# Optimization experiments

Hardware: AMD Instinct MI355X
Metric: run time of the kernel (lower is better)

## Reference

```python
import jax, jax.numpy as jnp
import numpy as np

N, D_IN, D_HID, D_OUT = 16384, 512, 2048, 512
NUM_BANDS, RANK, ALPHA = 4, 16, 32
SCALING = ALPHA / RANK  # 2.0


def setup_inputs() -> dict:
    key = jax.random.key(0)
    ks = jax.random.split(key, 10)
    x = jax.random.normal(ks[0], (N, D_IN), dtype=jnp.float32)
    bw = jax.random.uniform(ks[1], (N, NUM_BANDS), dtype=jnp.float32)
    band_weights = bw / jnp.sum(bw, axis=-1, keepdims=True)  # rows sum to 1
    s_in = 1.0 / np.sqrt(D_IN)
    s_hid = 1.0 / np.sqrt(D_HID)
    return {
        "x": x,
        "band_weights": band_weights,
        "W1": jax.random.normal(ks[2], (D_IN, D_HID), dtype=jnp.float32) * s_in,
        "b1": jax.random.normal(ks[3], (D_HID,), dtype=jnp.float32) * 0.01,
        "W2": jax.random.normal(ks[4], (D_HID, D_OUT), dtype=jnp.float32) * s_hid,
        "b2": jax.random.normal(ks[5], (D_OUT,), dtype=jnp.float32) * 0.01,
        "lora_fc1_A": jax.random.normal(ks[6], (NUM_BANDS, D_IN, RANK), dtype=jnp.float32) * s_in,
        "lora_fc1_B": jax.random.normal(ks[7], (NUM_BANDS, RANK, D_HID), dtype=jnp.float32) * 0.02,
        "lora_fc2_A": jax.random.normal(ks[8], (NUM_BANDS, D_HID, RANK), dtype=jnp.float32) * s_hid,
        "lora_fc2_B": jax.random.normal(ks[9], (NUM_BANDS, RANK, D_OUT), dtype=jnp.float32) * 0.02,
    }


def reference(x, band_weights, W1, b1, W2, b2, lora_fc1_A, lora_fc1_B, lora_fc2_A, lora_fc2_B):
    # shared fc1: [N, hidden]
    h_shared = x @ W1 + b1
    # per-band LoRA down-projection: [N, bands, rank]
    t1 = jnp.einsum('ni,bir->nbr', x, lora_fc1_A)
    # up-project and band-weighted sum fused: [N, hidden]
    delta1 = jnp.einsum('nb,nbr,brh->nh', band_weights, t1, lora_fc1_B) * SCALING
    h = jax.nn.gelu(h_shared + delta1, approximate=False)  # torch GELU is erf-based
    out_shared = h @ W2 + b2
    t2 = jnp.einsum('nh,bhr->nbr', h, lora_fc2_A)
    delta2 = jnp.einsum('nb,nbr,bro->no', band_weights, t2, lora_fc2_B) * SCALING
    return out_shared + delta2
```

## Files before the change

### kernel.cpp

```cpp
#include <hip/hip_runtime.h>
#include <hip/hip_bf16.h>

#define DEV __device__ __forceinline__
#define AS1 __attribute__((address_space(1)))
#define AS3 __attribute__((address_space(3)))

typedef __attribute__((ext_vector_type(8))) short bf16x8;
typedef __attribute__((ext_vector_type(4))) float f32x4;

static constexpr int NR   = 16384;
static constexpr int DIN  = 512;
static constexpr int DHID = 2048;
static constexpr int DOUT = 512;
static constexpr int LR   = 64;
static constexpr int K1   = DIN + LR;
static constexpr int K2   = DHID + LR;

DEV unsigned short f2bf(float f) {
  unsigned u = __float_as_uint(f);
  u += 0x7fffu + ((u >> 16) & 1u);
  return (unsigned short)(u >> 16);
}

DEV float fast_gelu(float v) {
  float x2 = v * v;
  float a  = -v * __builtin_fmaf(0.10294324f, x2, 2.30220817f);
  float t  = exp2f(a);
  return v * __builtin_amdgcn_rcpf(1.0f + t);
}

template<int N> DEV void wvm() {
  asm volatile("s_waitcnt vmcnt(%0)" :: "i"(N) : "memory");
}

__global__ __launch_bounds__(256) void cvt_x_kernel(const float* __restrict__ x,
                                                    unsigned short* __restrict__ xaug) {
  int i = blockIdx.x * 256 + threadIdx.x;
  if (i >= NR * DIN / 4) return;
  int e = i * 4;
  int r = e >> 9, c = e & 511;
  float4 v = ((const float4*)x)[i];
  uint2 o;
  o.x = (unsigned)f2bf(v.x) | ((unsigned)f2bf(v.y) << 16);
  o.y = (unsigned)f2bf(v.z) | ((unsigned)f2bf(v.w) << 16);
  *(uint2*)(xaug + (size_t)r * K1 + c) = o;
}

template<int R, int C, int LDO, int CO>
__global__ __launch_bounds__(256) void tconv_kernel(const float* __restrict__ in,
                                                    unsigned short* __restrict__ out) {
  __shared__ float t[32][33];
  int bc = blockIdx.x * 32, br = blockIdx.y * 32;
  int tx = threadIdx.x & 31, ty = threadIdx.x >> 5;
  #pragma unroll
  for (int i = 0; i < 32; i += 8)
    t[ty + i][tx] = in[(size_t)(br + ty + i) * C + bc + tx];
  __syncthreads();
  #pragma unroll
  for (int i = 0; i < 32; i += 8)
    out[(size_t)(bc + ty + i) * LDO + CO + br + tx] = f2bf(t[tx][ty + i]);
}

__global__ __launch_bounds__(256) void rearrA_kernel(const float* __restrict__ A,
                                                     unsigned short* __restrict__ AT, int D) {
  int tid = blockIdx.x * 256 + threadIdx.x;
  if (tid >= 64 * D) return;
  int j = tid / D, i = tid - j * D;
  AT[tid] = f2bf(A[((size_t)(j >> 4) * D + i) * 16 + (j & 15)]);
}

template<int BM, int BN, int WAVES, int K, int EPI>
__global__ __launch_bounds__(WAVES * 64, 2) void gemmx_kernel(
    const unsigned short* __restrict__ A, int lda,
    const unsigned short* __restrict__ B, int ldb,
    const float* __restrict__ bias,
    void* __restrict__ outp, int ldo, int ocol) {
  constexpr int THREADS = WAVES * 64;
  constexpr int NT = K / 64;
  constexpr int AL = BM * 4 / THREADS;
  constexpr int BL = BN * 4 / THREADS;
  constexpr int HA = (BM / 2) * 64;
  constexpr int HB = (BN / 2) * 64;
  constexpr int MQ = BM / 64;
  constexpr int WC = WAVES / 2;
  static_assert(NT >= 2 && AL == 2 && BL == 2, "geometry");
  __shared__ __align__(16) unsigned short lA[4 * HA];
  __shared__ __align__(16) unsigned short lB[4 * HB];

  const int tid  = threadIdx.x;
  const int w    = tid >> 6, lane = tid & 63;
  const int wr   = w / WC, wc = w % WC;
  const int bm   = blockIdx.x * BM, bn = blockIdx.y * BN;
  const int l15  = lane & 15;
  const int kc0  = ((lane >> 4) ^ (lane & 7)) * 8;
  const int kc1  = (((lane >> 4) + 4) ^ (lane & 7)) * 8;

  f32x4 acc[2][2][MQ][2] = {};
  bf16x8 af[2][MQ][2];
  bf16x8 bfv[2][2];

  auto stageA = [&](int buf, int half, int t) {
    #pragma unroll
    for (int i = 0; i < AL; ++i) {
      int row = w * (AL * 8) + i * 8 + (lane >> 3);
      __builtin_amdgcn_global_load_lds(
          (const AS1 void*)(A + (size_t)(bm + half * (BM / 2) + row) * lda
                              + (size_t)t * 64 + (((lane & 7) ^ (row & 7)) * 8)),
          (AS3 void*)(lA + (buf * 2 + half) * HA + (w * AL + i) * 512),
          16, 0, 0);
    }
  };
  auto stageB = [&](int buf, int half, int t) {
    #pragma unroll
    for (int i = 0; i < BL; ++i) {
      int row = w * (BL * 8) + i * 8 + (lane >> 3);
      __builtin_amdgcn_global_load_lds(
          (const AS1 void*)(B + (size_t)(bn + half * (BN / 2) + row) * ldb
                              + (size_t)t * 64 + (((lane & 7) ^ (row & 7)) * 8)),
          (AS3 void*)(lB + (buf * 2 + half) * HB + (w * BL + i) * 512),
          16, 0, 0);
    }
  };
  auto ldAall = [&](int buf) {
    #pragma unroll
    for (int mh = 0; mh < 2; ++mh) {
      const unsigned short* sA = lA + (buf * 2 + mh) * HA;
      #pragma unroll
      for (int m = 0; m < MQ; ++m) {
        int ro = (wr * (BM / 4) + m * 16 + l15) * 64;
        af[mh][m][0] = *(const bf16x8*)(sA + ro + kc0);
        af[mh][m][1] = *(const bf16x8*)(sA + ro + kc1);
      }
    }
  };
  auto ldB = [&](int buf, int nh) {
    const unsigned short* sB = lB + (buf * 2 + nh) * HB;
    #pragma unroll
    for (int n = 0; n < 2; ++n) {
      int ro = (wc * 32 + n * 16 + l15) * 64;
      bfv[n][0] = *(const bf16x8*)(sB + ro + kc0);
      bfv[n][1] = *(const bf16x8*)(sB + ro + kc1);
    }
  };

#define MFMA_Q(mh, nh)                                                           \
  __builtin_amdgcn_s_setprio(1);                                                 \
  _Pragma("unroll")                                                              \
  for (int m = 0; m < MQ; ++m)                                                   \
    _Pragma("unroll")                                                            \
    for (int n = 0; n < 2; ++n) {                                                \
      acc[mh][nh][m][n] = __builtin_amdgcn_mfma_f32_16x16x32_bf16(               \
          af[mh][m][0], bfv[n][0], acc[mh][nh][m][n], 0, 0, 0);                  \
      acc[mh][nh][m][n] = __builtin_amdgcn_mfma_f32_16x16x32_bf16(               \
          af[mh][m][1], bfv[n][1], acc[mh][nh][m][n], 0, 0, 0);                  \
    }                                                                            \
  __builtin_amdgcn_s_setprio(0);

#define BAR() __builtin_amdgcn_s_barrier()

  stageA(0, 0, 0); stageA(0, 1, 0); stageB(0, 0, 0); stageB(0, 1, 0);
  wvm<2>();
  BAR();

  for (int t = 0; t < NT; ++t) {
    const int buf = t & 1, nb = buf ^ 1;
    const bool more = (t + 1 < NT);
    ldAall(buf);
    ldB(buf, 0);
    if (more) { stageA(nb, 0, t + 1); stageA(nb, 1, t + 1); stageB(nb, 0, t + 1); }
    MFMA_Q(0, 0);
    MFMA_Q(1, 0);
    if (more) wvm<6>(); else wvm<0>();
    BAR();
    if (more) stageB(nb, 1, t + 1);
    ldB(buf, 1);
    MFMA_Q(0, 1);
    MFMA_Q(1, 1);
    if (more) {
      wvm<2>();
      BAR();
    }
  }
#undef MFMA_Q
#undef BAR

  float biasv[2][2];
  #pragma unroll
  for (int nh = 0; nh < 2; ++nh)
    #pragma unroll
    for (int n = 0; n < 2; ++n)
      biasv[nh][n] = bias[bn + nh * (BN / 2) + wc * 32 + n * 16 + l15];

  #pragma unroll
  for (int mh = 0; mh < 2; ++mh)
    #pragma unroll
    for (int nh = 0; nh < 2; ++nh)
      #pragma unroll
      for (int m = 0; m < MQ; ++m)
        #pragma unroll
        for (int n = 0; n < 2; ++n) {
          int col  = bn + nh * (BN / 2) + wc * 32 + n * 16 + l15;
          int rowb = bm + mh * (BM / 2) + wr * (BM / 4) + m * 16 + ((lane >> 4) << 2);
          #pragma unroll
          for (int r = 0; r < 4; ++r) {
            float v = acc[mh][nh][m][n][r];
            int row = rowb + r;
            if (EPI == 0) {
              v = fast_gelu(v + biasv[nh][n]);
              ((unsigned short*)outp)[(size_t)row * ldo + ocol + col] = f2bf(v);
            } else {
              v += biasv[nh][n];
              ((float*)outp)[(size_t)row * ldo + col] = v;
            }
          }
        }
}

template<int BM, int BN, int WM, int WN, int K>
__global__ __launch_bounds__(256) void gemmu_kernel(
    const unsigned short* __restrict__ A, int lda,
    const unsigned short* __restrict__ B, int ldb,
    const float* __restrict__ bw,
    unsigned short* __restrict__ outp, int ldo, int ocol) {
  constexpr int WRM = WM / 16, WRN = WN / 16;
  constexpr int NWN = BN / WN;
  constexpr int NT  = K / 64;
  constexpr int NBUF = 3;
  constexpr int AISS = BM * 64 * 2 / 4096;
  constexpr int BISS = BN * 64 * 2 / 4096;
  constexpr int LOADS = AISS + BISS;
  static_assert((BM / WM) * (BN / WN) == 4 && NT >= NBUF, "geometry");
  __shared__ __align__(16) unsigned short lA[NBUF * BM * 64];
  __shared__ __align__(16) unsigned short lB[NBUF * BN * 64];

  const int tid  = threadIdx.x;
  const int wid  = tid >> 6, lane = tid & 63;
  const int wr   = wid / NWN, wc = wid % NWN;
  const int bm   = blockIdx.x * BM, bn = blockIdx.y * BN;
  const int l15  = lane & 15;
  const int kc0  = ((lane >> 4) ^ (lane & 7)) * 8;
  const int kc1  = (((lane >> 4) + 4) ^ (lane & 7)) * 8;

  f32x4 acc[WRM][WRN] = {};

  auto stage = [&](int buf, int t) {
    #pragma unroll
    for (int i = 0; i < AISS; i++) {
      int row = (wid * AISS + i) * 8 + (lane >> 3);
      __builtin_amdgcn_global_load_lds(
          (const AS1 void*)(A + (size_t)(bm + row) * lda + (size_t)t * 64
                              + (((lane & 7) ^ (row & 7)) * 8)),
          (AS3 void*)(lA + buf * (BM * 64) + (wid * AISS + i) * 512), 16, 0, 0);
    }
    #pragma unroll
    for (int i = 0; i < BISS; i++) {
      int row = (wid * BISS + i) * 8 + (lane >> 3);
      __builtin_amdgcn_global_load_lds(
          (const AS1 void*)(B + (size_t)(bn + row) * ldb + (size_t)t * 64
                              + (((lane & 7) ^ (row & 7)) * 8)),
          (AS3 void*)(lB + buf * (BN * 64) + (wid * BISS + i) * 512), 16, 0, 0);
    }
  };
  auto compute = [&](int buf) {
    const unsigned short* pA = lA + buf * (BM * 64);
    const unsigned short* pB = lB + buf * (BN * 64);
    bf16x8 af[WRM][2], bfv[WRN][2];
    #pragma unroll
    for (int m = 0; m < WRM; m++) {
      int ro = (wr * WM + m * 16 + l15) * 64;
      af[m][0] = *(const bf16x8*)(pA + ro + kc0);
      af[m][1] = *(const bf16x8*)(pA + ro + kc1);
    }
    #pragma unroll
    for (int n = 0; n < WRN; n++) {
      int ro = (wc * WN + n * 16 + l15) * 64;
      bfv[n][0] = *(const bf16x8*)(pB + ro + kc0);
      bfv[n][1] = *(const bf16x8*)(pB + ro + kc1);
    }
    #pragma unroll
    for (int m = 0; m < WRM; m++)
      #pragma unroll
      for (int n = 0; n < WRN; n++) {
        acc[m][n] = __builtin_amdgcn_mfma_f32_16x16x32_bf16(af[m][0], bfv[n][0], acc[m][n], 0, 0, 0);
        acc[m][n] = __builtin_amdgcn_mfma_f32_16x16x32_bf16(af[m][1], bfv[n][1], acc[m][n], 0, 0, 0);
      }
  };

  stage(0, 0); stage(1, 1); stage(2, 2);
  wvm<2 * LOADS>();
  __builtin_amdgcn_s_barrier();

  int bt = 0;
  for (int t = 0; t < NT; ++t) {
    compute(bt);
    __builtin_amdgcn_s_barrier();
    if (t + 1 < NT) {
      if (t + NBUF < NT) stage(bt, t + NBUF);
      int newer = (t + NBUF < NT) ? (NBUF - 1) : (NT - 2 - t);
      if (newer >= 2)      wvm<2 * LOADS>();
      else if (newer == 1) wvm<LOADS>();
      else                 wvm<0>();
      __builtin_amdgcn_s_barrier();
      bt = (bt == NBUF - 1) ? 0 : bt + 1;
    }
  }

  const int r0 = bm + wr * WM;
  const int c0 = bn + wc * WN;
  #pragma unroll
  for (int m = 0; m < WRM; m++)
    #pragma unroll
    for (int n = 0; n < WRN; n++) {
      int col  = c0 + n * 16 + l15;
      int rowb = r0 + m * 16 + ((lane >> 4) << 2);
      #pragma unroll
      for (int r = 0; r < 4; r++) {
        float v = acc[m][n][r] * 2.0f * bw[(rowb + r) * 4 + (col >> 4)];
        outp[(size_t)(rowb + r) * ldo + ocol + col] = f2bf(v);
      }
    }
}

extern "C" void kernel_launch(void* const* d_in, const int* in_sizes, int n_in,
                              void* d_out, int out_size, void* d_ws, size_t ws_size,
                              hipStream_t stream) {
  const float* x  = (const float*)d_in[0];
  const float* bw = (const float*)d_in[1];
  const float* W1 = (const float*)d_in[2];
  const float* b1 = (const float*)d_in[3];
  const float* W2 = (const float*)d_in[4];
  const float* b2 = (const float*)d_in[5];
  const float* A1 = (const float*)d_in[6];
  const float* B1 = (const float*)d_in[7];
  const float* A2 = (const float*)d_in[8];
  const float* B2 = (const float*)d_in[9];
  float* out = (float*)d_out;

  char* w = (char*)d_ws;
  unsigned short* xaug = (unsigned short*)w;  w += (size_t)NR * K1 * 2;
  unsigned short* haug = (unsigned short*)w;  w += (size_t)NR * K2 * 2;
  unsigned short* W1cT = (unsigned short*)w;  w += (size_t)DHID * K1 * 2;
  unsigned short* W2cT = (unsigned short*)w;  w += (size_t)DOUT * K2 * 2;
  unsigned short* A1T  = (unsigned short*)w;  w += (size_t)64 * DIN * 2;
  unsigned short* A2T  = (unsigned short*)w;  w += (size_t)64 * DHID * 2;

  cvt_x_kernel<<<NR * DIN / 4 / 256, 256, 0, stream>>>(x, xaug);
  tconv_kernel<512, 2048, K1, 0><<<dim3(64, 16), 256, 0, stream>>>(W1, W1cT);
  tconv_kernel<64, 2048, K1, 512><<<dim3(64, 2), 256, 0, stream>>>(B1, W1cT);
  tconv_kernel<2048, 512, K2, 0><<<dim3(16, 64), 256, 0, stream>>>(W2, W2cT);
  tconv_kernel<64, 512, K2, 2048><<<dim3(16, 2), 256, 0, stream>>>(B2, W2cT);
  rearrA_kernel<<<128, 256, 0, stream>>>(A1, A1T, 512);
  rearrA_kernel<<<512, 256, 0, stream>>>(A2, A2T, 2048);

  gemmu_kernel<64, 64, 32, 32, 512><<<dim3(NR / 64, 1), 256, 0, stream>>>(
      xaug, K1, A1T, DIN, bw, xaug, K1, 512);
  gemmx_kernel<256, 256, 8, K1, 0><<<dim3(NR / 256, DHID / 256), 512, 0, stream>>>(
      xaug, K1, W1cT, K1, b1, haug, K2, 0);
  gemmu_kernel<64, 64, 32, 32, 2048><<<dim3(NR / 64, 1), 256, 0, stream>>>(
      haug, K2, A2T, DHID, bw, haug, K2, 2048);
  gemmx_kernel<128, 128, 4, K2, 1><<<dim3(NR / 128, DOUT / 128), 256, 0, stream>>>(
      haug, K2, W2cT, K2, b2, out, DOUT, 0);
}
```

Baseline: 145.0 us.

## Merge weight prep kernels, fuse x conversion into LoRA down-projection, retile fc2 GEMM

```diff
diff --git a/kernel.cpp b/kernel.cpp
--- a/kernel.cpp
+++ b/kernel.cpp
@@ -33,25 +33,10 @@
   asm volatile("s_waitcnt vmcnt(%0)" :: "i"(N) : "memory");
 }
 
-__global__ __launch_bounds__(256) void cvt_x_kernel(const float* __restrict__ x,
-                                                    unsigned short* __restrict__ xaug) {
-  int i = blockIdx.x * 256 + threadIdx.x;
-  if (i >= NR * DIN / 4) return;
-  int e = i * 4;
-  int r = e >> 9, c = e & 511;
-  float4 v = ((const float4*)x)[i];
-  uint2 o;
-  o.x = (unsigned)f2bf(v.x) | ((unsigned)f2bf(v.y) << 16);
-  o.y = (unsigned)f2bf(v.z) | ((unsigned)f2bf(v.w) << 16);
-  *(uint2*)(xaug + (size_t)r * K1 + c) = o;
-}
-
-template<int R, int C, int LDO, int CO>
-__global__ __launch_bounds__(256) void tconv_kernel(const float* __restrict__ in,
-                                                    unsigned short* __restrict__ out) {
-  __shared__ float t[32][33];
-  int bc = blockIdx.x * 32, br = blockIdx.y * 32;
-  int tx = threadIdx.x & 31, ty = threadIdx.x >> 5;
+DEV void tconv_dev(const float* in, unsigned short* out, int C, int LDO, int CO,
+                   int bx, int by, float (*t)[33], int tid) {
+  int bc = bx * 32, br = by * 32;
+  int tx = tid & 31, ty = tid >> 5;
   #pragma unroll
   for (int i = 0; i < 32; i += 8)
     t[ty + i][tx] = in[(size_t)(br + ty + i) * C + bc + tx];
@@ -61,12 +46,94 @@
     out[(size_t)(bc + ty + i) * LDO + CO + br + tx] = f2bf(t[tx][ty + i]);
 }
 
-__global__ __launch_bounds__(256) void rearrA_kernel(const float* __restrict__ A,
-                                                     unsigned short* __restrict__ AT, int D) {
-  int tid = blockIdx.x * 256 + threadIdx.x;
-  if (tid >= 64 * D) return;
-  int j = tid / D, i = tid - j * D;
-  AT[tid] = f2bf(A[((size_t)(j >> 4) * D + i) * 16 + (j & 15)]);
+__global__ __launch_bounds__(256) void prep_kernel(
+    const float* __restrict__ W1, const float* __restrict__ B1,
+    const float* __restrict__ W2, const float* __restrict__ B2,
+    unsigned short* __restrict__ W1cT, unsigned short* __restrict__ W2cT,
+    const float* __restrict__ A1, const float* __restrict__ A2,
+    unsigned short* __restrict__ A1T, unsigned short* __restrict__ A2T) {
+  __shared__ float t[32][33];
+  const int b = blockIdx.x, tid = threadIdx.x;
+  if (b < 1024) {
+    tconv_dev(W1, W1cT, 2048, K1, 0, b & 63, b >> 6, t, tid);
+  } else if (b < 2048) {
+    int bi = b - 1024;
+    tconv_dev(W2, W2cT, 512, K2, 0, bi & 15, bi >> 4, t, tid);
+  } else if (b < 2176) {
+    int bi = b - 2048;
+    tconv_dev(B1, W1cT, 2048, K1, 512, bi & 63, bi >> 6, t, tid);
+  } else if (b < 2208) {
+    int bi = b - 2176;
+    tconv_dev(B2, W2cT, 512, K2, 2048, bi & 15, bi >> 4, t, tid);
+  } else if (b < 2336) {
+    int i2 = (b - 2208) * 256 + tid;
+    int j = i2 / DIN, i = i2 - j * DIN;
+    A1T[i2] = f2bf(A1[((size_t)(j >> 4) * DIN + i) * 16 + (j & 15)]);
+  } else {
+    int i2 = (b - 2336) * 256 + tid;
+    int j = i2 / DHID, i = i2 - j * DHID;
+    A2T[i2] = f2bf(A2[((size_t)(j >> 4) * DHID + i) * 16 + (j & 15)]);
+  }
+}
+
+__global__ __launch_bounds__(256) void u1cvt_kernel(
+    const float* __restrict__ x, const float* __restrict__ bw,
+    const unsigned short* __restrict__ A1T, unsigned short* __restrict__ xaug) {
+  __shared__ __align__(16) unsigned short lX[64 * 64];
+  __shared__ __align__(16) unsigned short lW[64 * 64];
+  const int tid = threadIdx.x;
+  const int w = tid >> 6, lane = tid & 63;
+  const int bm = blockIdx.x * 64;
+  const int l15 = lane & 15;
+  const int kc0 = ((lane >> 4) ^ (lane & 7)) * 8;
+  const int kc1 = (((lane >> 4) + 4) ^ (lane & 7)) * 8;
+
+  f32x4 acc[4] = {};
+
+  for (int kt = 0; kt < 8; ++kt) {
+    #pragma unroll
+    for (int i = 0; i < 2; ++i) {
+      int row = i * 32 + w * 8 + (lane >> 3);
+      __builtin_amdgcn_global_load_lds(
+          (const AS1 void*)(A1T + (size_t)row * DIN + kt * 64
+                              + (((lane & 7) ^ (row & 7)) * 8)),
+          (AS3 void*)(lW + (i * 32 + w * 8) * 64 + lane * 8), 16, 0, 0);
+    }
+    #pragma unroll
+    for (int p = 0; p < 4; ++p) {
+      int row = p * 16 + (tid >> 4);
+      int col = (tid & 15) * 4;
+      float4 v = *(const float4*)(x + (size_t)(bm + row) * DIN + kt * 64 + col);
+      uint2 o;
+      o.x = (unsigned)f2bf(v.x) | ((unsigned)f2bf(v.y) << 16);
+      o.y = (unsigned)f2bf(v.z) | ((unsigned)f2bf(v.w) << 16);
+      *(uint2*)(xaug + (size_t)(bm + row) * K1 + kt * 64 + col) = o;
+      char* p3 = (char*)lX + row * 128 + (((col >> 3) ^ (row & 7)) << 4) + ((col & 7) << 1);
+      *(uint2*)p3 = o;
+    }
+    __syncthreads();
+    bf16x8 af0 = *(const bf16x8*)(lX + (w * 16 + l15) * 64 + kc0);
+    bf16x8 af1 = *(const bf16x8*)(lX + (w * 16 + l15) * 64 + kc1);
+    #pragma unroll
+    for (int n = 0; n < 4; ++n) {
+      bf16x8 b0 = *(const bf16x8*)(lW + (n * 16 + l15) * 64 + kc0);
+      bf16x8 b1 = *(const bf16x8*)(lW + (n * 16 + l15) * 64 + kc1);
+      acc[n] = __builtin_amdgcn_mfma_f32_16x16x32_bf16(af0, b0, acc[n], 0, 0, 0);
+      acc[n] = __builtin_amdgcn_mfma_f32_16x16x32_bf16(af1, b1, acc[n], 0, 0, 0);
+    }
+    __syncthreads();
+  }
+
+  #pragma unroll
+  for (int n = 0; n < 4; ++n) {
+    int col = n * 16 + l15;
+    #pragma unroll
+    for (int r = 0; r < 4; ++r) {
+      int row = bm + w * 16 + ((lane >> 4) << 2) + r;
+      float v = acc[n][r] * 2.0f * bw[row * 4 + n];
+      xaug[(size_t)row * K1 + 512 + col] = f2bf(v);
+    }
+  }
 }
 
 template<int BM, int BN, int WAVES, int K, int EPI>
@@ -83,7 +150,7 @@
   constexpr int HB = (BN / 2) * 64;
   constexpr int MQ = BM / 64;
   constexpr int WC = WAVES / 2;
-  static_assert(NT >= 2 && AL == 2 && BL == 2, "geometry");
+  static_assert(NT >= 2 && AL >= 1 && BL >= 1 && (BN / 2) / WC == 32, "geometry");
   __shared__ __align__(16) unsigned short lA[4 * HA];
   __shared__ __align__(16) unsigned short lB[4 * HB];
 
@@ -159,7 +226,7 @@
 #define BAR() __builtin_amdgcn_s_barrier()
 
   stageA(0, 0, 0); stageA(0, 1, 0); stageB(0, 0, 0); stageB(0, 1, 0);
-  wvm<2>();
+  wvm<BL>();
   BAR();
 
   for (int t = 0; t < NT; ++t) {
@@ -170,14 +237,14 @@
     if (more) { stageA(nb, 0, t + 1); stageA(nb, 1, t + 1); stageB(nb, 0, t + 1); }
     MFMA_Q(0, 0);
     MFMA_Q(1, 0);
-    if (more) wvm<6>(); else wvm<0>();
+    if (more) wvm<2 * AL + BL>(); else wvm<0>();
     BAR();
     if (more) stageB(nb, 1, t + 1);
     ldB(buf, 1);
     MFMA_Q(0, 1);
     MFMA_Q(1, 1);
     if (more) {
-      wvm<2>();
+      wvm<BL>();
       BAR();
     }
   }
@@ -344,20 +411,12 @@
   unsigned short* A1T  = (unsigned short*)w;  w += (size_t)64 * DIN * 2;
   unsigned short* A2T  = (unsigned short*)w;  w += (size_t)64 * DHID * 2;
 
-  cvt_x_kernel<<<NR * DIN / 4 / 256, 256, 0, stream>>>(x, xaug);
-  tconv_kernel<512, 2048, K1, 0><<<dim3(64, 16), 256, 0, stream>>>(W1, W1cT);
-  tconv_kernel<64, 2048, K1, 512><<<dim3(64, 2), 256, 0, stream>>>(B1, W1cT);
-  tconv_kernel<2048, 512, K2, 0><<<dim3(16, 64), 256, 0, stream>>>(W2, W2cT);
-  tconv_kernel<64, 512, K2, 2048><<<dim3(16, 2), 256, 0, stream>>>(B2, W2cT);
-  rearrA_kernel<<<128, 256, 0, stream>>>(A1, A1T, 512);
-  rearrA_kernel<<<512, 256, 0, stream>>>(A2, A2T, 2048);
-
-  gemmu_kernel<64, 64, 32, 32, 512><<<dim3(NR / 64, 1), 256, 0, stream>>>(
-      xaug, K1, A1T, DIN, bw, xaug, K1, 512);
+  prep_kernel<<<2848, 256, 0, stream>>>(W1, B1, W2, B2, W1cT, W2cT, A1, A2, A1T, A2T);
+  u1cvt_kernel<<<NR / 64, 256, 0, stream>>>(x, bw, A1T, xaug);
   gemmx_kernel<256, 256, 8, K1, 0><<<dim3(NR / 256, DHID / 256), 512, 0, stream>>>(
       xaug, K1, W1cT, K1, b1, haug, K2, 0);
   gemmu_kernel<64, 64, 32, 32, 2048><<<dim3(NR / 64, 1), 256, 0, stream>>>(
       haug, K2, A2T, DHID, bw, haug, K2, 2048);
-  gemmx_kernel<128, 128, 4, K2, 1><<<dim3(NR / 128, DOUT / 128), 256, 0, stream>>>(
+  gemmx_kernel<128, 256, 8, K2, 1><<<dim3(NR / 128, DOUT / 256), 512, 0, stream>>>(
       haug, K2, W2cT, K2, b2, out, DOUT, 0);
 }
```

Measured after the change: 139.5 us. 3.8% less time.
